# Kernel tuning notes

Measured on AMD Instinct MI355X. Metric: run time of the kernel, lower is better.

The kernel has to match this reference:

```python
import jax, jax.numpy as jnp
import numpy as np


def setup_inputs() -> dict:
    key = jax.random.key(0)
    kq, kk, kv = jax.random.split(key, 3)
    B, H, S, D = 2, 16, 2048, 64
    q = jax.random.normal(kq, (B, H, S, D), dtype=jnp.float32)
    k = jax.random.normal(kk, (B, H, S, D), dtype=jnp.float32)
    v = jax.random.normal(kv, (B, H, S, D), dtype=jnp.float32)
    return {"q": q, "k": k, "v": v}


def reference(q, k, v):
    # Tiled attention without online softmax computes the same math as
    # standard scaled dot-product attention (non-causal).
    D = q.shape[-1]
    scale = 1.0 / jnp.sqrt(jnp.asarray(D, dtype=q.dtype))
    # scores: [B, H, Sq, Sk]
    scores = jnp.einsum("bhqd,bhkd->bhqk", q, k) * scale
    attn = jax.nn.softmax(scores, axis=-1)
    out = jnp.einsum("bhqk,bhkd->bhqd", attn, v)
    return out
```

## Files before the change

### kernel.cpp

```cpp
#include <hip/hip_runtime.h>
#include <hip/hip_bf16.h>
#include <stdint.h>


#define B_ 2
#define H_ 16
#define S_ 2048
#define D_ 64
#define BH_ (B_ * H_)
#define QBLK 128
#define KVBLK 64
#define NKV (S_ / KVBLK)
#define NPER (NKV / 2)

typedef __bf16 bf16_t;
typedef bf16_t bf16x8 __attribute__((ext_vector_type(8)));
typedef bf16_t bf16x4 __attribute__((ext_vector_type(4)));
typedef float f32x16 __attribute__((ext_vector_type(16)));
typedef uint32_t u32;

__device__ __forceinline__ f32x16 mfma32(bf16x8 a, bf16x8 b, f32x16 c) {
  return __builtin_amdgcn_mfma_f32_32x32x16_bf16(a, b, c, 0, 0, 0);
}

__device__ __forceinline__ u32 cvt_pk_bf16(float lo, float hi) {
  u32 r;
  asm("v_cvt_pk_bf16_f32 %0, %1, %2" : "=v"(r) : "v"(lo), "v"(hi));
  return r;
}

__device__ __forceinline__ void swap32(u32& x, u32& y) {
  asm("v_permlane32_swap_b32 %0, %1" : "+v"(x), "+v"(y));
}

__device__ __forceinline__ void gload_lds16(const bf16_t* g, bf16_t* l) {
  __builtin_amdgcn_global_load_lds(
      (const __attribute__((address_space(1))) unsigned int*)g,
      (__attribute__((address_space(3))) unsigned int*)l, 16, 0, 0);
}

__global__ void prepass_kernel(const float* __restrict__ k,
                               const float* __restrict__ v,
                               bf16_t* __restrict__ kb,
                               bf16_t* __restrict__ vt) {
  __shared__ float tile[64][65];
  const int bh = blockIdx.y, kt = blockIdx.x;
  if (blockIdx.z == 0) {
    const float* src = k + ((size_t)bh * S_ + (size_t)kt * 64) * D_;
    bf16_t* dst = kb + ((size_t)bh * S_ + (size_t)kt * 64) * D_;
#pragma unroll
    for (int i = 0; i < 4; ++i) {
      int idx = i * 256 + threadIdx.x;
      float4 x = ((const float4*)src)[idx];
      bf16x4 o = { (bf16_t)x.x, (bf16_t)x.y, (bf16_t)x.z, (bf16_t)x.w };
      *(bf16x4*)(dst + (size_t)idx * 4) = o;
    }
  } else {
    const float* vp = v + ((size_t)bh * S_ + (size_t)kt * 64) * D_;
    int r0 = threadIdx.x >> 4;
    int c4 = (threadIdx.x & 15) * 4;
#pragma unroll
    for (int p = 0; p < 4; ++p) {
      int r = r0 + p * 16;
      float4 x = *(const float4*)(vp + (size_t)r * D_ + c4);
      tile[r][c4 + 0] = x.x; tile[r][c4 + 1] = x.y;
      tile[r][c4 + 2] = x.z; tile[r][c4 + 3] = x.w;
    }
    __syncthreads();
    bf16_t* op = vt + (size_t)bh * D_ * S_ + (size_t)kt * 64;
#pragma unroll
    for (int p = 0; p < 4; ++p) {
      int d = r0 + p * 16;
      bf16x4 o = { (bf16_t)tile[c4 + 0][d], (bf16_t)tile[c4 + 1][d],
                   (bf16_t)tile[c4 + 2][d], (bf16_t)tile[c4 + 3][d] };
      *(bf16x4*)(op + (size_t)d * S_ + c4) = o;
    }
  }
}

__global__ __launch_bounds__(512, 4) void attn_kernel(
    const float* __restrict__ q, const bf16_t* __restrict__ kb,
    const bf16_t* __restrict__ vt, float* __restrict__ out) {
  const int bid = blockIdx.x;
  const int g = bid >> 3;
  const int bh = 4 * (bid & 7) + (g >> 4);
  const int qt = g & 15;
  const int tid = threadIdx.x;
  const int wid = tid >> 6;
  const int lane = tid & 63;
  const int wq = wid & 3;
  const int wkv = wid >> 2;
  const int l31 = lane & 31;
  const int hi = lane >> 5;

  __shared__ __align__(16) char smem[65536];
  bf16_t* kbuf = (bf16_t*)smem;
  bf16_t* vbuf = (bf16_t*)(smem + 32768);
  float* epi = (float*)smem;

  const bf16_t* kp = kb + (size_t)bh * S_ * D_;
  const bf16_t* vp = vt + (size_t)bh * D_ * S_;

  const int srow = tid >> 3;
  const int scol = (tid & 7) ^ (srow & 7);
  const int kofs = srow * D_ + scol * 8;
  const size_t vofs = (size_t)srow * S_ + scol * 8;
  const int ldst = wid * 512;

  const float qscale = 0.125f * 1.4426950408889634f;
  const int qrow = qt * QBLK + wq * 32 + l31;
  const float* qpr = q + ((size_t)bh * S_ + qrow) * D_;
  bf16x8 bq[4];
#pragma unroll
  for (int ks = 0; ks < 4; ++ks) {
    const float* p = qpr + ks * 16 + hi * 8;
    float4 x0 = *(const float4*)(p);
    float4 x1 = *(const float4*)(p + 4);
    bf16x8 a;
    a[0] = (bf16_t)(x0.x * qscale); a[1] = (bf16_t)(x0.y * qscale);
    a[2] = (bf16_t)(x0.z * qscale); a[3] = (bf16_t)(x0.w * qscale);
    a[4] = (bf16_t)(x1.x * qscale); a[5] = (bf16_t)(x1.y * qscale);
    a[6] = (bf16_t)(x1.z * qscale); a[7] = (bf16_t)(x1.w * qscale);
    bq[ks] = a;
  }

  float lsum = 0.f;
  f32x16 o0, o1;
#pragma unroll
  for (int r = 0; r < 16; ++r) { o0[r] = 0.f; o1[r] = 0.f; }

#pragma unroll
  for (int par = 0; par < 2; ++par) {
    gload_lds16(kp + (size_t)par * (KVBLK * D_) + kofs, kbuf + par * 4096 + ldst);
    gload_lds16(vp + (size_t)par * KVBLK + vofs, vbuf + par * 4096 + ldst);
  }
  __syncthreads();

  for (int p = 0; p < NPER; ++p) {
    if (p + 1 < NPER) {
      const int nb = ((p + 1) & 1) * 2;
#pragma unroll
      for (int par = 0; par < 2; ++par) {
        const int t = 2 * p + 2 + par;
        gload_lds16(kp + (size_t)t * (KVBLK * D_) + kofs,
                    kbuf + (nb + par) * 4096 + ldst);
        gload_lds16(vp + (size_t)t * KVBLK + vofs,
                    vbuf + (nb + par) * 4096 + ldst);
      }
    }

    const bf16_t* kt_ = kbuf + ((p & 1) * 2 + wkv) * 4096;
    const bf16_t* vt_ = vbuf + ((p & 1) * 2 + wkv) * 4096;

    u32 w[2][8];
#pragma unroll
    for (int sub = 0; sub < 2; ++sub) {
      f32x16 sv;
#pragma unroll
      for (int r = 0; r < 16; ++r) sv[r] = 0.f;
#pragma unroll
      for (int ks = 0; ks < 4; ++ks) {
        const int row = sub * 32 + l31;
        const int ch = (2 * ks + hi) ^ (row & 7);
        bf16x8 a = *(const bf16x8*)(kt_ + row * D_ + ch * 8);
        sv = mfma32(a, bq[ks], sv);
      }
#pragma unroll
      for (int b = 0; b < 4; ++b) {
        float e0 = __builtin_amdgcn_exp2f(sv[4 * b + 0]);
        float e1 = __builtin_amdgcn_exp2f(sv[4 * b + 1]);
        float e2 = __builtin_amdgcn_exp2f(sv[4 * b + 2]);
        float e3 = __builtin_amdgcn_exp2f(sv[4 * b + 3]);
        lsum += (e0 + e1) + (e2 + e3);
        w[sub][2 * b + 0] = cvt_pk_bf16(e0, e1);
        w[sub][2 * b + 1] = cvt_pk_bf16(e2, e3);
      }
#pragma unroll
      for (int kt2 = 0; kt2 < 2; ++kt2) {
        swap32(w[sub][4 * kt2 + 0], w[sub][4 * kt2 + 2]);
        swap32(w[sub][4 * kt2 + 1], w[sub][4 * kt2 + 3]);
      }
    }

#pragma unroll
    for (int sub = 0; sub < 2; ++sub)
#pragma unroll
      for (int kt2 = 0; kt2 < 2; ++kt2) {
        union { u32 u[4]; bf16x8 v; } pb;
        pb.u[0] = w[sub][4 * kt2 + 0]; pb.u[1] = w[sub][4 * kt2 + 1];
        pb.u[2] = w[sub][4 * kt2 + 2]; pb.u[3] = w[sub][4 * kt2 + 3];
        {
          const int row = l31;
          const int ch = (4 * sub + 2 * kt2 + hi) ^ (row & 7);
          bf16x8 a = *(const bf16x8*)(vt_ + row * KVBLK + ch * 8);
          o0 = mfma32(a, pb.v, o0);
        }
        {
          const int row = 32 + l31;
          const int ch = (4 * sub + 2 * kt2 + hi) ^ (row & 7);
          bf16x8 a = *(const bf16x8*)(vt_ + row * KVBLK + ch * 8);
          o1 = mfma32(a, pb.v, o1);
        }
      }

    __syncthreads();
  }

  if (wkv == 1) {
    float* e = epi + ((size_t)wq * 64 + lane) * 33;
#pragma unroll
    for (int r = 0; r < 16; ++r) { e[r] = o0[r]; e[16 + r] = o1[r]; }
    e[32] = lsum;
  }
  __syncthreads();
  if (wkv == 0) {
    const float* e = epi + ((size_t)wq * 64 + lane) * 33;
#pragma unroll
    for (int r = 0; r < 16; ++r) { o0[r] += e[r]; o1[r] += e[16 + r]; }
    lsum += e[32];
    float ltot = lsum + __shfl_xor(lsum, 32, 64);
    float inv = 1.f / ltot;
    float* op = out + ((size_t)bh * S_ + qrow) * D_;
#pragma unroll
    for (int b = 0; b < 4; ++b) {
      float4 w0 = { o0[4 * b + 0] * inv, o0[4 * b + 1] * inv,
                    o0[4 * b + 2] * inv, o0[4 * b + 3] * inv };
      *(float4*)(op + 8 * b + 4 * hi) = w0;
      float4 w1 = { o1[4 * b + 0] * inv, o1[4 * b + 1] * inv,
                    o1[4 * b + 2] * inv, o1[4 * b + 3] * inv };
      *(float4*)(op + 32 + 8 * b + 4 * hi) = w1;
    }
  }
}

extern "C" void kernel_launch(void* const* d_in, const int* in_sizes, int n_in,
                              void* d_out, int out_size, void* d_ws, size_t ws_size,
                              hipStream_t stream) {
  const float* q = (const float*)d_in[0];
  const float* k = (const float*)d_in[1];
  const float* v = (const float*)d_in[2];
  float* out = (float*)d_out;

  bf16_t* kb = (bf16_t*)d_ws;
  bf16_t* vt = kb + (size_t)BH_ * S_ * D_;

  prepass_kernel<<<dim3(S_ / 64, BH_, 2), 256, 0, stream>>>(k, v, kb, vt);
  attn_kernel<<<dim3(BH_ * (S_ / QBLK)), 512, 0, stream>>>(q, kb, vt, out);
}
```

Baseline: 55.76 us.

## Fuse K fp32-to-bf16 conversion into attention kernel's K tile loads

The prepass no longer converts K to bf16. Instead the attention kernel loads fp32 K tiles from global memory into registers, converts them to bf16, and writes them swizzled into LDS after the PV MFMAs, replacing the async global_load_lds path for K. This removes one prepass write and re-read of K, at the cost of reading twice the bytes of K from global memory in every block (16 q-tiles per head) and adding register pressure and VALU conversion work inside the main loop.

```diff
diff --git a/kernel.cpp b/kernel.cpp
--- a/kernel.cpp
+++ b/kernel.cpp
@@ -39,47 +39,33 @@
       (__attribute__((address_space(3))) unsigned int*)l, 16, 0, 0);
 }
 
-__global__ void prepass_kernel(const float* __restrict__ k,
-                               const float* __restrict__ v,
-                               bf16_t* __restrict__ kb,
+__global__ void prepass_kernel(const float* __restrict__ v,
                                bf16_t* __restrict__ vt) {
   __shared__ float tile[64][65];
   const int bh = blockIdx.y, kt = blockIdx.x;
-  if (blockIdx.z == 0) {
-    const float* src = k + ((size_t)bh * S_ + (size_t)kt * 64) * D_;
-    bf16_t* dst = kb + ((size_t)bh * S_ + (size_t)kt * 64) * D_;
-#pragma unroll
-    for (int i = 0; i < 4; ++i) {
-      int idx = i * 256 + threadIdx.x;
-      float4 x = ((const float4*)src)[idx];
-      bf16x4 o = { (bf16_t)x.x, (bf16_t)x.y, (bf16_t)x.z, (bf16_t)x.w };
-      *(bf16x4*)(dst + (size_t)idx * 4) = o;
-    }
-  } else {
-    const float* vp = v + ((size_t)bh * S_ + (size_t)kt * 64) * D_;
-    int r0 = threadIdx.x >> 4;
-    int c4 = (threadIdx.x & 15) * 4;
-#pragma unroll
-    for (int p = 0; p < 4; ++p) {
-      int r = r0 + p * 16;
-      float4 x = *(const float4*)(vp + (size_t)r * D_ + c4);
-      tile[r][c4 + 0] = x.x; tile[r][c4 + 1] = x.y;
-      tile[r][c4 + 2] = x.z; tile[r][c4 + 3] = x.w;
-    }
-    __syncthreads();
-    bf16_t* op = vt + (size_t)bh * D_ * S_ + (size_t)kt * 64;
-#pragma unroll
-    for (int p = 0; p < 4; ++p) {
-      int d = r0 + p * 16;
-      bf16x4 o = { (bf16_t)tile[c4 + 0][d], (bf16_t)tile[c4 + 1][d],
-                   (bf16_t)tile[c4 + 2][d], (bf16_t)tile[c4 + 3][d] };
-      *(bf16x4*)(op + (size_t)d * S_ + c4) = o;
-    }
+  const float* vp = v + ((size_t)bh * S_ + (size_t)kt * 64) * D_;
+  int r0 = threadIdx.x >> 4;
+  int c4 = (threadIdx.x & 15) * 4;
+#pragma unroll
+  for (int p = 0; p < 4; ++p) {
+    int r = r0 + p * 16;
+    float4 x = *(const float4*)(vp + (size_t)r * D_ + c4);
+    tile[r][c4 + 0] = x.x; tile[r][c4 + 1] = x.y;
+    tile[r][c4 + 2] = x.z; tile[r][c4 + 3] = x.w;
+  }
+  __syncthreads();
+  bf16_t* op = vt + (size_t)bh * D_ * S_ + (size_t)kt * 64;
+#pragma unroll
+  for (int p = 0; p < 4; ++p) {
+    int d = r0 + p * 16;
+    bf16x4 o = { (bf16_t)tile[c4 + 0][d], (bf16_t)tile[c4 + 1][d],
+                 (bf16_t)tile[c4 + 2][d], (bf16_t)tile[c4 + 3][d] };
+    *(bf16x4*)(op + (size_t)d * S_ + c4) = o;
   }
 }
 
 __global__ __launch_bounds__(512, 4) void attn_kernel(
-    const float* __restrict__ q, const bf16_t* __restrict__ kb,
+    const float* __restrict__ q, const float* __restrict__ kf,
     const bf16_t* __restrict__ vt, float* __restrict__ out) {
   const int bid = blockIdx.x;
   const int g = bid >> 3;
@@ -98,13 +84,15 @@
   bf16_t* vbuf = (bf16_t*)(smem + 32768);
   float* epi = (float*)smem;
 
-  const bf16_t* kp = kb + (size_t)bh * S_ * D_;
+  const float* kp32 = kf + (size_t)bh * S_ * D_;
   const bf16_t* vp = vt + (size_t)bh * D_ * S_;
 
   const int srow = tid >> 3;
-  const int scol = (tid & 7) ^ (srow & 7);
-  const int kofs = srow * D_ + scol * 8;
-  const size_t vofs = (size_t)srow * S_ + scol * 8;
+  const int scol = tid & 7;
+  const int kofs32 = srow * D_ + scol * 8;
+  const int kwofs = srow * D_ + ((scol ^ (srow & 7)) * 8);
+  const int vscol = scol ^ (srow & 7);
+  const size_t vofs = (size_t)srow * S_ + vscol * 8;
   const int ldst = wid * 512;
 
   const float qscale = 0.125f * 1.4426950408889634f;
@@ -131,19 +119,30 @@
 
 #pragma unroll
   for (int par = 0; par < 2; ++par) {
-    gload_lds16(kp + (size_t)par * (KVBLK * D_) + kofs, kbuf + par * 4096 + ldst);
+    const float* kg = kp32 + (size_t)par * (KVBLK * D_) + kofs32;
+    float4 x0 = *(const float4*)(kg);
+    float4 x1 = *(const float4*)(kg + 4);
+    bf16x8 kb8;
+    kb8[0] = (bf16_t)x0.x; kb8[1] = (bf16_t)x0.y;
+    kb8[2] = (bf16_t)x0.z; kb8[3] = (bf16_t)x0.w;
+    kb8[4] = (bf16_t)x1.x; kb8[5] = (bf16_t)x1.y;
+    kb8[6] = (bf16_t)x1.z; kb8[7] = (bf16_t)x1.w;
+    *(bf16x8*)(kbuf + par * 4096 + kwofs) = kb8;
     gload_lds16(vp + (size_t)par * KVBLK + vofs, vbuf + par * 4096 + ldst);
   }
   __syncthreads();
 
   for (int p = 0; p < NPER; ++p) {
+    float4 kx00, kx01, kx10, kx11;
+    const int nb = ((p + 1) & 1) * 2;
     if (p + 1 < NPER) {
-      const int nb = ((p + 1) & 1) * 2;
+      const float* kg0 = kp32 + (size_t)(2 * p + 2) * (KVBLK * D_) + kofs32;
+      const float* kg1 = kp32 + (size_t)(2 * p + 3) * (KVBLK * D_) + kofs32;
+      kx00 = *(const float4*)(kg0); kx01 = *(const float4*)(kg0 + 4);
+      kx10 = *(const float4*)(kg1); kx11 = *(const float4*)(kg1 + 4);
 #pragma unroll
       for (int par = 0; par < 2; ++par) {
         const int t = 2 * p + 2 + par;
-        gload_lds16(kp + (size_t)t * (KVBLK * D_) + kofs,
-                    kbuf + (nb + par) * 4096 + ldst);
         gload_lds16(vp + (size_t)t * KVBLK + vofs,
                     vbuf + (nb + par) * 4096 + ldst);
       }
@@ -203,6 +202,20 @@
         }
       }
 
+    if (p + 1 < NPER) {
+      bf16x8 kb8;
+      kb8[0] = (bf16_t)kx00.x; kb8[1] = (bf16_t)kx00.y;
+      kb8[2] = (bf16_t)kx00.z; kb8[3] = (bf16_t)kx00.w;
+      kb8[4] = (bf16_t)kx01.x; kb8[5] = (bf16_t)kx01.y;
+      kb8[6] = (bf16_t)kx01.z; kb8[7] = (bf16_t)kx01.w;
+      *(bf16x8*)(kbuf + nb * 4096 + kwofs) = kb8;
+      kb8[0] = (bf16_t)kx10.x; kb8[1] = (bf16_t)kx10.y;
+      kb8[2] = (bf16_t)kx10.z; kb8[3] = (bf16_t)kx10.w;
+      kb8[4] = (bf16_t)kx11.x; kb8[5] = (bf16_t)kx11.y;
+      kb8[6] = (bf16_t)kx11.z; kb8[7] = (bf16_t)kx11.w;
+      *(bf16x8*)(kbuf + (nb + 1) * 4096 + kwofs) = kb8;
+    }
+
     __syncthreads();
   }
 
@@ -241,9 +254,8 @@
   const float* v = (const float*)d_in[2];
   float* out = (float*)d_out;
 
-  bf16_t* kb = (bf16_t*)d_ws;
-  bf16_t* vt = kb + (size_t)BH_ * S_ * D_;
-
-  prepass_kernel<<<dim3(S_ / 64, BH_, 2), 256, 0, stream>>>(k, v, kb, vt);
-  attn_kernel<<<dim3(BH_ * (S_ / QBLK)), 512, 0, stream>>>(q, kb, vt, out);
-}
+  bf16_t* vt = (bf16_t*)d_ws;
+
+  prepass_kernel<<<dim3(S_ / 64, BH_), 256, 0, stream>>>(v, vt);
+  attn_kernel<<<dim3(BH_ * (S_ / QBLK)), 512, 0, stream>>>(q, k, vt, out);
+}
```

Result: slower. 68.03 us (+22.0%).

## Software-pipeline PV of previous tile with QK and exp of current tile

Applied to the files above, without the earlier changes.

Restructures the main loop so that each iteration computes QK^T for the current KV tile, then the PV MFMAs for the previous tile's probabilities, then the exp/pack for the current tile, with a tail PV after the loop. V loads are shifted one stage behind K loads so that each V tile arrives in time for its delayed consumption. The intent is to let matrix-core work overlap the transcendental/VALU softmax work and hide latency. It costs more live registers (two score accumulators plus the carried probabilities), which may pressure occupancy at 512 threads x 4 blocks.

```diff
diff --git a/kernel.cpp b/kernel.cpp
--- a/kernel.cpp
+++ b/kernel.cpp
@@ -130,41 +130,68 @@
   for (int r = 0; r < 16; ++r) { o0[r] = 0.f; o1[r] = 0.f; }
 
 #pragma unroll
-  for (int par = 0; par < 2; ++par) {
+  for (int par = 0; par < 2; ++par)
     gload_lds16(kp + (size_t)par * (KVBLK * D_) + kofs, kbuf + par * 4096 + ldst);
-    gload_lds16(vp + (size_t)par * KVBLK + vofs, vbuf + par * 4096 + ldst);
-  }
   __syncthreads();
 
-  for (int p = 0; p < NPER; ++p) {
-    if (p + 1 < NPER) {
-      const int nb = ((p + 1) & 1) * 2;
-#pragma unroll
-      for (int par = 0; par < 2; ++par) {
-        const int t = 2 * p + 2 + par;
-        gload_lds16(kp + (size_t)t * (KVBLK * D_) + kofs,
+  u32 wp[2][8];
+
+  for (int i = 0; i < NPER; ++i) {
+    if (i + 1 < NPER) {
+      const int nb = ((i + 1) & 1) * 2;
+#pragma unroll
+      for (int par = 0; par < 2; ++par)
+        gload_lds16(kp + (size_t)(2 * (i + 1) + par) * (KVBLK * D_) + kofs,
                     kbuf + (nb + par) * 4096 + ldst);
-        gload_lds16(vp + (size_t)t * KVBLK + vofs,
-                    vbuf + (nb + par) * 4096 + ldst);
-      }
-    }
-
-    const bf16_t* kt_ = kbuf + ((p & 1) * 2 + wkv) * 4096;
-    const bf16_t* vt_ = vbuf + ((p & 1) * 2 + wkv) * 4096;
-
-    u32 w[2][8];
+    }
+    {
+      const int vb = (i & 1) * 2;
+#pragma unroll
+      for (int par = 0; par < 2; ++par)
+        gload_lds16(vp + (size_t)(2 * i + par) * KVBLK + vofs,
+                    vbuf + (vb + par) * 4096 + ldst);
+    }
+
+    const bf16_t* kt_ = kbuf + ((i & 1) * 2 + wkv) * 4096;
+
+    f32x16 sv0, sv1;
+#pragma unroll
+    for (int r = 0; r < 16; ++r) { sv0[r] = 0.f; sv1[r] = 0.f; }
+#pragma unroll
+    for (int ks = 0; ks < 4; ++ks) {
+      const int row0 = l31;
+      const int ch0 = (2 * ks + hi) ^ (row0 & 7);
+      bf16x8 a0 = *(const bf16x8*)(kt_ + row0 * D_ + ch0 * 8);
+      sv0 = mfma32(a0, bq[ks], sv0);
+      const int row1 = 32 + l31;
+      const int ch1 = (2 * ks + hi) ^ (row1 & 7);
+      bf16x8 a1 = *(const bf16x8*)(kt_ + row1 * D_ + ch1 * 8);
+      sv1 = mfma32(a1, bq[ks], sv1);
+    }
+
+    if (i > 0) {
+      const bf16_t* vt_ = vbuf + (((i + 1) & 1) * 2 + wkv) * 4096;
+#pragma unroll
+      for (int sub = 0; sub < 2; ++sub)
+#pragma unroll
+        for (int kt2 = 0; kt2 < 2; ++kt2) {
+          union { u32 u[4]; bf16x8 v; } pb;
+          pb.u[0] = wp[sub][4 * kt2 + 0]; pb.u[1] = wp[sub][4 * kt2 + 1];
+          pb.u[2] = wp[sub][4 * kt2 + 2]; pb.u[3] = wp[sub][4 * kt2 + 3];
+          const int row = l31;
+          const int ch = (4 * sub + 2 * kt2 + hi) ^ (row & 7);
+          bf16x8 a = *(const bf16x8*)(vt_ + row * KVBLK + ch * 8);
+          o0 = mfma32(a, pb.v, o0);
+          const int rowb = 32 + l31;
+          const int chb = (4 * sub + 2 * kt2 + hi) ^ (rowb & 7);
+          bf16x8 ab = *(const bf16x8*)(vt_ + rowb * KVBLK + chb * 8);
+          o1 = mfma32(ab, pb.v, o1);
+        }
+    }
+
 #pragma unroll
     for (int sub = 0; sub < 2; ++sub) {
-      f32x16 sv;
-#pragma unroll
-      for (int r = 0; r < 16; ++r) sv[r] = 0.f;
-#pragma unroll
-      for (int ks = 0; ks < 4; ++ks) {
-        const int row = sub * 32 + l31;
-        const int ch = (2 * ks + hi) ^ (row & 7);
-        bf16x8 a = *(const bf16x8*)(kt_ + row * D_ + ch * 8);
-        sv = mfma32(a, bq[ks], sv);
-      }
+      const f32x16 sv = sub ? sv1 : sv0;
 #pragma unroll
       for (int b = 0; b < 4; ++b) {
         float e0 = __builtin_amdgcn_exp2f(sv[4 * b + 0]);
@@ -172,38 +199,37 @@
         float e2 = __builtin_amdgcn_exp2f(sv[4 * b + 2]);
         float e3 = __builtin_amdgcn_exp2f(sv[4 * b + 3]);
         lsum += (e0 + e1) + (e2 + e3);
-        w[sub][2 * b + 0] = cvt_pk_bf16(e0, e1);
-        w[sub][2 * b + 1] = cvt_pk_bf16(e2, e3);
+        wp[sub][2 * b + 0] = cvt_pk_bf16(e0, e1);
+        wp[sub][2 * b + 1] = cvt_pk_bf16(e2, e3);
       }
 #pragma unroll
       for (int kt2 = 0; kt2 < 2; ++kt2) {
-        swap32(w[sub][4 * kt2 + 0], w[sub][4 * kt2 + 2]);
-        swap32(w[sub][4 * kt2 + 1], w[sub][4 * kt2 + 3]);
+        swap32(wp[sub][4 * kt2 + 0], wp[sub][4 * kt2 + 2]);
+        swap32(wp[sub][4 * kt2 + 1], wp[sub][4 * kt2 + 3]);
       }
     }
 
+    __syncthreads();
+  }
+
+  {
+    const bf16_t* vt_ = vbuf + (2 + wkv) * 4096;
 #pragma unroll
     for (int sub = 0; sub < 2; ++sub)
 #pragma unroll
       for (int kt2 = 0; kt2 < 2; ++kt2) {
         union { u32 u[4]; bf16x8 v; } pb;
-        pb.u[0] = w[sub][4 * kt2 + 0]; pb.u[1] = w[sub][4 * kt2 + 1];
-        pb.u[2] = w[sub][4 * kt2 + 2]; pb.u[3] = w[sub][4 * kt2 + 3];
-        {
-          const int row = l31;
-          const int ch = (4 * sub + 2 * kt2 + hi) ^ (row & 7);
-          bf16x8 a = *(const bf16x8*)(vt_ + row * KVBLK + ch * 8);
-          o0 = mfma32(a, pb.v, o0);
-        }
-        {
-          const int row = 32 + l31;
-          const int ch = (4 * sub + 2 * kt2 + hi) ^ (row & 7);
-          bf16x8 a = *(const bf16x8*)(vt_ + row * KVBLK + ch * 8);
-          o1 = mfma32(a, pb.v, o1);
-        }
+        pb.u[0] = wp[sub][4 * kt2 + 0]; pb.u[1] = wp[sub][4 * kt2 + 1];
+        pb.u[2] = wp[sub][4 * kt2 + 2]; pb.u[3] = wp[sub][4 * kt2 + 3];
+        const int row = l31;
+        const int ch = (4 * sub + 2 * kt2 + hi) ^ (row & 7);
+        bf16x8 a = *(const bf16x8*)(vt_ + row * KVBLK + ch * 8);
+        o0 = mfma32(a, pb.v, o0);
+        const int rowb = 32 + l31;
+        const int chb = (4 * sub + 2 * kt2 + hi) ^ (rowb & 7);
+        bf16x8 ab = *(const bf16x8*)(vt_ + rowb * KVBLK + chb * 8);
+        o1 = mfma32(ab, pb.v, o1);
       }
-
-    __syncthreads();
   }
 
   if (wkv == 1) {
```

Measured after the change: 56.13 us. About the same (+0.7%).
